# Kernel optimization log

Measured on AMD Instinct MI355X. Metric: run time of the kernel, lower is better.

## Reference

```python
import jax, jax.numpy as jnp
import numpy as np

EPS = 1e-5  # BatchNorm eps (eval mode, running stats mean=0, var=1)
BN_SCALE = 1.0 / np.sqrt(1.0 + EPS)


def setup_inputs() -> dict:
    key = jax.random.key(0)
    ks = jax.random.split(key, 5)
    N, T, C, V, K = 64, 300, 64, 25, 3
    x = jax.random.normal(ks[0], (N, T, C, V), dtype=jnp.float32)
    # G: Linear(T -> 2T, no bias), Linear(2T -> K, no bias)
    g_w1 = jax.random.normal(ks[1], (2 * T, T), dtype=jnp.float32) * (1.0 / np.sqrt(T))
    g_w2 = jax.random.normal(ks[2], (K, 2 * T), dtype=jnp.float32) * (1.0 / np.sqrt(2 * T))
    # L: Conv1d(C -> C//4, K, pad=K//2, no bias), Conv1d(C//4 -> C, 1, no bias)
    l_w1 = jax.random.normal(ks[3], (C // 4, C, K), dtype=jnp.float32) * (1.0 / np.sqrt(C * K))
    l_w2 = jax.random.normal(ks[4], (C, C // 4), dtype=jnp.float32) * (1.0 / np.sqrt(C // 4))
    return {"x": x, "g_w1": g_w1, "g_w2": g_w2, "l_w1": l_w1, "l_w2": l_w2}


def reference(x, g_w1, g_w2, l_w1, l_w2):
    # x: [N, T, C, V]; n_segment == T so n_batch == N
    N, T, C, V = x.shape
    K = g_w2.shape[0]
    pad = K // 2
    # new_x: [N, C, T, V]
    new_x = jnp.transpose(x, (0, 2, 1, 3))
    # adaptive avg pool over V -> [N, C, T]
    pooled = jnp.mean(new_x, axis=-1)

    # --- G branch: per-(n,c) temporal kernel of size K ---
    g_in = pooled.reshape(N * C, T)                         # [N*C, T]
    h = jnp.maximum(g_in @ g_w1.T * BN_SCALE, 0.0)          # Linear + BN(eval) + ReLU
    conv_kernel = jax.nn.softmax(h @ g_w2.T, axis=-1)       # [N*C, K]
    conv_kernel = conv_kernel.reshape(N, C, K)

    # --- L branch: local activation over time ---
    z = jax.lax.conv_general_dilated(
        pooled, l_w1, window_strides=(1,), padding=[(pad, pad)],
        dimension_numbers=("NCH", "OIH", "NCH"))              # [N, C//4, T]
    z = jnp.maximum(z * BN_SCALE, 0.0)
    local_act = jax.nn.sigmoid(jnp.einsum("nct,oc->not", z, l_w2))  # [N, C, T]

    new_x = new_x * local_act[..., None]                    # [N, C, T, V]

    # --- per-(n,c) depthwise temporal conv (groups = N*C) ---
    xpad = jnp.pad(new_x, ((0, 0), (0, 0), (pad, pad), (0, 0)))
    windows = jnp.stack([xpad[:, :, k:k + T, :] for k in range(K)], axis=-1)  # [N,C,T,V,K]
    out = jnp.einsum("nctvk,nck->nctv", windows, conv_kernel)

    return jnp.transpose(out, (0, 2, 1, 3))                 # [N, T, C, V]
```

## Files before the change

### kernel.cpp

```cpp
#include <hip/hip_runtime.h>
#include <hip/hip_bf16.h>
#include <math.h>

#define BN_SCALE_F 0.99999500003749969f

typedef short short8v __attribute__((ext_vector_type(8)));
typedef float float4v __attribute__((ext_vector_type(4)));


__global__ __launch_bounds__(256) void pool_prep_kernel(const float* __restrict__ x,
                                                        const float* __restrict__ g_w1,
                                                        const float* __restrict__ l_w1,
                                                        float* __restrict__ pooled,
                                                        __hip_bfloat16* __restrict__ pooledb,
                                                        __hip_bfloat16* __restrict__ w1b,
                                                        float* __restrict__ lw1r) {
  __shared__ float buf[6400];
  int bid = blockIdx.x;
  if (bid < 4800) {
    const float4* src = (const float4*)(x + (size_t)bid * 6400);
    float4* b4 = (float4*)buf;
    for (int i = threadIdx.x; i < 1600; i += 256) b4[i] = src[i];
    __syncthreads();
    int wave = threadIdx.x >> 6;
    int c = threadIdx.x & 63;
    int nt = bid * 4 + wave;
    int n = nt / 300, t = nt - n * 300;
    const float* p = buf + wave * 1600 + c * 25;
    float s = 0.f;
#pragma unroll
    for (int v = 0; v < 25; ++v) s += p[v];
    float pv = s * 0.04f;
    size_t row = (size_t)(n * 64 + c);
    pooled[row * 300 + t] = pv;
    pooledb[row * 320 + t] = __float2bfloat16(pv);
  } else if (bid < 4816) {
    int b = bid - 4800;
    for (int i = b * 256 + threadIdx.x; i < 608 * 320; i += 16 * 256) {
      int j = i / 320, k = i - j * 320;
      float v = (j < 600 && k < 300) ? g_w1[(size_t)j * 300 + k] : 0.f;
      w1b[i] = __float2bfloat16(v);
    }
  } else if (bid == 4816) {
    for (int i = threadIdx.x; i < 4096 * 20; i += 256) {
      int row = i / 20, k = 300 + (i - row * 20);
      pooledb[(size_t)row * 320 + k] = __float2bfloat16(0.f);
    }
  } else {
    for (int i = threadIdx.x; i < 3072; i += 256) {
      int o = i / 192;
      int rem = i - o * 192;
      int c = rem / 3;
      int k = rem - c * 3;
      lw1r[c * 48 + o * 3 + k] = l_w1[i];
    }
  }
}

union GLSmem {
  struct {
    float hbuf[16][612];
    float logits[48];
  } g;
  struct {
    float p[64][80];
    float z[75][20];
  } l;
};

__global__ __launch_bounds__(320) void gl_kernel(const float* __restrict__ pooled,
                                                 const __hip_bfloat16* __restrict__ pooledb,
                                                 const __hip_bfloat16* __restrict__ w1b,
                                                 const float* __restrict__ g_w2,
                                                 const float* __restrict__ lw1r,
                                                 const float* __restrict__ l_w2,
                                                 float* __restrict__ kern,
                                                 float* __restrict__ la) {
  __shared__ GLSmem sm;
  int bid = blockIdx.x;
  int tid = threadIdx.x;
  int wave = tid >> 6, lane = tid & 63;
  if (bid < 256) {
    int r0 = bid * 16;
    int row16 = lane & 15;
    int k8 = (lane >> 4) * 8;

    float4v acc[8];
#pragma unroll
    for (int q = 0; q < 8; ++q) acc[q] = (float4v){0.f, 0.f, 0.f, 0.f};

    const short* pa = (const short*)pooledb + (size_t)(r0 + row16) * 320 + k8;
    const short* pb = (const short*)w1b + k8;

    for (int kt = 0; kt < 10; ++kt) {
      short8v av = *(const short8v*)(pa + kt * 32);
#pragma unroll
      for (int q = 0; q < 8; ++q) {
        int jt = wave + 5 * q;
        if (jt < 38) {
          short8v bv = *(const short8v*)(pb + (size_t)(jt * 16 + row16) * 320 + kt * 32);
          acc[q] = __builtin_amdgcn_mfma_f32_16x16x32_bf16(av, bv, acc[q], 0, 0, 0);
        }
      }
    }

#pragma unroll
    for (int q = 0; q < 8; ++q) {
      int jt = wave + 5 * q;
      if (jt < 38) {
        int col = jt * 16 + row16;
#pragma unroll
        for (int reg = 0; reg < 4; ++reg) {
          int i = (lane >> 4) * 4 + reg;
          sm.g.hbuf[i][col] = fmaxf(acc[q][reg] * BN_SCALE_F, 0.f);
        }
      }
    }
    __syncthreads();

    for (int o = wave; o < 48; o += 5) {
      int r = o / 3, k = o - r * 3;
      float s = 0.f;
#pragma unroll
      for (int q = 0; q < 10; ++q) {
        int jj = lane + q * 64;
        if (jj < 600) s = fmaf(sm.g.hbuf[r][jj], g_w2[k * 600 + jj], s);
      }
#pragma unroll
      for (int off = 1; off < 64; off <<= 1) s += __shfl_xor(s, off, 64);
      if (lane == 0) sm.g.logits[o] = s;
    }
    __syncthreads();
    if (tid < 16) {
      float a = sm.g.logits[tid * 3 + 0];
      float b = sm.g.logits[tid * 3 + 1];
      float c = sm.g.logits[tid * 3 + 2];
      float m = fmaxf(a, fmaxf(b, c));
      float ea = expf(a - m), eb = expf(b - m), ec = expf(c - m);
      float inv = 1.f / (ea + eb + ec);
      size_t o = (size_t)(r0 + tid) * 3;
      kern[o] = ea * inv;
      kern[o + 1] = eb * inv;
      kern[o + 2] = ec * inv;
    }
  } else {
    int bid2 = bid - 256;
    int n = bid2 >> 2;
    int tc = bid2 & 3;
    int t0 = tc * 75;
    for (int i = tid; i < 64 * 77; i += 320) {
      int c = i / 77, tt = i - c * 77;
      int gt = t0 - 1 + tt;
      sm.l.p[c][tt] = (gt >= 0 && gt < 300) ? pooled[(size_t)(n * 64 + c) * 300 + gt] : 0.f;
    }
    __syncthreads();
    {
      int og = tid / 80;
      int tl = tid - og * 80;
      if (tl < 75) {
        float acc[4] = {0.f, 0.f, 0.f, 0.f};
        for (int c = 0; c < 64; ++c) {
          const float* wr = lw1r + c * 48 + og * 12;
          float pk0 = sm.l.p[c][tl];
          float pk1 = sm.l.p[c][tl + 1];
          float pk2 = sm.l.p[c][tl + 2];
#pragma unroll
          for (int oi = 0; oi < 4; ++oi) {
            acc[oi] = fmaf(wr[oi * 3 + 0], pk0, acc[oi]);
            acc[oi] = fmaf(wr[oi * 3 + 1], pk1, acc[oi]);
            acc[oi] = fmaf(wr[oi * 3 + 2], pk2, acc[oi]);
          }
        }
        float4 zv;
        zv.x = fmaxf(acc[0] * BN_SCALE_F, 0.f);
        zv.y = fmaxf(acc[1] * BN_SCALE_F, 0.f);
        zv.z = fmaxf(acc[2] * BN_SCALE_F, 0.f);
        zv.w = fmaxf(acc[3] * BN_SCALE_F, 0.f);
        *(float4*)(&sm.l.z[tl][og * 4]) = zv;
      }
    }
    __syncthreads();
    {
      int c = tid / 5;
      int ts = tid - c * 5;
      const float4* w2v = (const float4*)(l_w2 + c * 16);
      float4 wA = w2v[0], wB = w2v[1], wC = w2v[2], wD = w2v[3];
      float* outp = la + (size_t)(n * 64 + c) * 300 + t0;
      for (int it = 0; it < 15; ++it) {
        int tl = ts + it * 5;
        const float4* zv = (const float4*)(&sm.l.z[tl][0]);
        float4 zA = zv[0], zB = zv[1], zC = zv[2], zD = zv[3];
        float s = zA.x * wA.x + zA.y * wA.y + zA.z * wA.z + zA.w * wA.w;
        s += zB.x * wB.x + zB.y * wB.y + zB.z * wB.z + zB.w * wB.w;
        s += zC.x * wC.x + zC.y * wC.y + zC.z * wC.z + zC.w * wC.w;
        s += zD.x * wD.x + zD.y * wD.y + zD.z * wD.z + zD.w * wD.w;
        outp[tl] = 1.f / (1.f + expf(-s));
      }
    }
  }
}

__global__ __launch_bounds__(256) void tam_final_kernel(const float* __restrict__ x,
                                                        const float* __restrict__ la,
                                                        const float* __restrict__ kern,
                                                        float* __restrict__ out) {
  int bid = blockIdx.x;
  int n = bid >> 4;
  int rem = bid & 15;
  int tch = rem >> 1;
  int half = rem & 1;
  int cv4 = half * 256 + threadIdx.x;
  if (cv4 >= 400) return;
  int e0 = cv4 * 4;
  int c0 = e0 / 25;
  int c3 = (e0 + 3) / 25;
  bool s1 = ((e0 + 1) / 25) != c0;
  bool s2 = ((e0 + 2) / 25) != c0;
  bool s3 = (c3 != c0);
  const float* lap0 = la + (size_t)(n * 64 + c0) * 300;
  const float* lap1 = la + (size_t)(n * 64 + c3) * 300;
  const float* kp0 = kern + (size_t)(n * 64 + c0) * 3;
  const float* kp1 = kern + (size_t)(n * 64 + c3) * 3;
  float k00 = kp0[0], k01 = kp0[1], k02 = kp0[2];
  float k10 = kp1[0], k11 = kp1[1], k12 = kp1[2];
  float4 K0 = {k00, s1 ? k10 : k00, s2 ? k10 : k00, s3 ? k10 : k00};
  float4 K1 = {k01, s1 ? k11 : k01, s2 ? k11 : k01, s3 ? k11 : k01};
  float4 K2 = {k02, s1 ? k12 : k02, s2 ? k12 : k02, s3 ? k12 : k02};

  const float4* xp = (const float4*)(x + (size_t)n * 480000) + cv4;
  float4* op = (float4*)(out + (size_t)n * 480000) + cv4;

  int t0 = tch * 38;
  int tend = t0 + 38;
  if (tend > 300) tend = 300;

#define LAMUL(dst, t)                                        \
  {                                                          \
    float l0 = lap0[(t)];                                    \
    float l1 = lap1[(t)];                                    \
    float4 xv = xp[(size_t)(t) * 400];                       \
    dst.x = xv.x * l0;                                       \
    dst.y = xv.y * (s1 ? l1 : l0);                           \
    dst.z = xv.z * (s2 ? l1 : l0);                           \
    dst.w = xv.w * (s3 ? l1 : l0);                           \
  }

  float4 am, ac, an;
  if (t0 > 0) {
    LAMUL(am, t0 - 1);
  } else {
    am = {0.f, 0.f, 0.f, 0.f};
  }
  LAMUL(ac, t0);
  for (int t = t0; t < tend; ++t) {
    if (t + 1 < 300) {
      LAMUL(an, t + 1);
    } else {
      an = {0.f, 0.f, 0.f, 0.f};
    }
    float4 o;
    o.x = fmaf(am.x, K0.x, fmaf(ac.x, K1.x, an.x * K2.x));
    o.y = fmaf(am.y, K0.y, fmaf(ac.y, K1.y, an.y * K2.y));
    o.z = fmaf(am.z, K0.z, fmaf(ac.z, K1.z, an.z * K2.z));
    o.w = fmaf(am.w, K0.w, fmaf(ac.w, K1.w, an.w * K2.w));
    op[(size_t)t * 400] = o;
    am = ac;
    ac = an;
  }
#undef LAMUL
}

extern "C" void kernel_launch(void* const* d_in, const int* in_sizes, int n_in,
                              void* d_out, int out_size, void* d_ws, size_t ws_size,
                              hipStream_t stream) {
  const float* x = (const float*)d_in[0];
  const float* g_w1 = (const float*)d_in[1];
  const float* g_w2 = (const float*)d_in[2];
  const float* l_w1 = (const float*)d_in[3];
  const float* l_w2 = (const float*)d_in[4];
  float* out = (float*)d_out;
  float* ws = (float*)d_ws;
  float* pooled = ws;
  float* kern = ws + 1228800;
  float* lact = ws + 1228800 + 12288;
  __hip_bfloat16* pooledb = (__hip_bfloat16*)(ws + 2469888);
  __hip_bfloat16* w1b = (__hip_bfloat16*)(ws + 2469888 + 655360);
  float* lw1r = ws + 2469888 + 655360 + 97280;

  hipLaunchKernelGGL(pool_prep_kernel, dim3(4818), dim3(256), 0, stream, x, g_w1, l_w1,
                     pooled, pooledb, w1b, lw1r);
  hipLaunchKernelGGL(gl_kernel, dim3(512), dim3(320), 0, stream, pooled, pooledb, w1b,
                     g_w2, lw1r, l_w2, kern, lact);
  hipLaunchKernelGGL(tam_final_kernel, dim3(1024), dim3(256), 0, stream, x, lact, kern, out);
}
```

Measured before the change: 121.2 us.

## Write pooled activations in time-major layout and transpose to bf16 in separate kernel

The pooling kernel now writes pooled values contiguously as [N,T,C] (coalesced across channels) instead of strided scatter stores into [N*C,T] fp32 and bf16 buffers. A new prep kernel transposes this through shared memory into the padded bf16 layout used by the G-branch matmul, zeroing the pad columns as part of the tile. It also converts the weights. The L branch reads the time-major layout directly, and its shared tile is padded to 81 columns to avoid bank conflicts. This targets uncoalesced global stores, at the cost of an extra kernel launch and an extra pass over the pooled data.

Result: faster. 112.3 us (-7.3%).

```diff
diff --git a/kernel.cpp b/kernel.cpp
--- a/kernel.cpp
+++ b/kernel.cpp
@@ -8,43 +8,50 @@
 typedef float float4v __attribute__((ext_vector_type(4)));
 
 
-__global__ __launch_bounds__(256) void pool_prep_kernel(const float* __restrict__ x,
-                                                        const float* __restrict__ g_w1,
-                                                        const float* __restrict__ l_w1,
-                                                        float* __restrict__ pooled,
-                                                        __hip_bfloat16* __restrict__ pooledb,
-                                                        __hip_bfloat16* __restrict__ w1b,
-                                                        float* __restrict__ lw1r) {
+__global__ __launch_bounds__(256) void pool_kernel(const float* __restrict__ x,
+                                                   float* __restrict__ pooledT) {
   __shared__ float buf[6400];
   int bid = blockIdx.x;
-  if (bid < 4800) {
-    const float4* src = (const float4*)(x + (size_t)bid * 6400);
-    float4* b4 = (float4*)buf;
-    for (int i = threadIdx.x; i < 1600; i += 256) b4[i] = src[i];
-    __syncthreads();
-    int wave = threadIdx.x >> 6;
-    int c = threadIdx.x & 63;
-    int nt = bid * 4 + wave;
-    int n = nt / 300, t = nt - n * 300;
-    const float* p = buf + wave * 1600 + c * 25;
-    float s = 0.f;
-#pragma unroll
-    for (int v = 0; v < 25; ++v) s += p[v];
-    float pv = s * 0.04f;
-    size_t row = (size_t)(n * 64 + c);
-    pooled[row * 300 + t] = pv;
-    pooledb[row * 320 + t] = __float2bfloat16(pv);
-  } else if (bid < 4816) {
-    int b = bid - 4800;
+  const float4* src = (const float4*)(x + (size_t)bid * 6400);
+  float4* b4 = (float4*)buf;
+  for (int i = threadIdx.x; i < 1600; i += 256) b4[i] = src[i];
+  __syncthreads();
+  int wave = threadIdx.x >> 6;
+  int c = threadIdx.x & 63;
+  const float* p = buf + wave * 1600 + c * 25;
+  float s = 0.f;
+#pragma unroll
+  for (int v = 0; v < 25; ++v) s += p[v];
+  pooledT[(size_t)(bid * 4 + wave) * 64 + c] = s * 0.04f;
+}
+
+__global__ __launch_bounds__(256) void prep2_kernel(const float* __restrict__ pooledT,
+                                                    const float* __restrict__ g_w1,
+                                                    const float* __restrict__ l_w1,
+                                                    __hip_bfloat16* __restrict__ pooledb,
+                                                    __hip_bfloat16* __restrict__ w1b,
+                                                    float* __restrict__ lw1r) {
+  int bid = blockIdx.x;
+  if (bid < 320) {
+    __shared__ float tile[64][65];
+    int n = bid / 5;
+    int tt0 = (bid % 5) * 64;
+    for (int i = threadIdx.x; i < 4096; i += 256) {
+      int tt = i >> 6, c = i & 63;
+      int t = tt0 + tt;
+      tile[tt][c] = (t < 300) ? pooledT[((size_t)n * 300 + t) * 64 + c] : 0.f;
+    }
+    __syncthreads();
+    for (int i = threadIdx.x; i < 4096; i += 256) {
+      int c = i >> 6, tt = i & 63;
+      pooledb[((size_t)(n * 64 + c)) * 320 + tt0 + tt] = __float2bfloat16(tile[tt][c]);
+    }
+  } else if (bid < 336) {
+    int b = bid - 320;
     for (int i = b * 256 + threadIdx.x; i < 608 * 320; i += 16 * 256) {
       int j = i / 320, k = i - j * 320;
       float v = (j < 600 && k < 300) ? g_w1[(size_t)j * 300 + k] : 0.f;
       w1b[i] = __float2bfloat16(v);
-    }
-  } else if (bid == 4816) {
-    for (int i = threadIdx.x; i < 4096 * 20; i += 256) {
-      int row = i / 20, k = 300 + (i - row * 20);
-      pooledb[(size_t)row * 320 + k] = __float2bfloat16(0.f);
     }
   } else {
     for (int i = threadIdx.x; i < 3072; i += 256) {
@@ -63,12 +70,12 @@
     float logits[48];
   } g;
   struct {
-    float p[64][80];
+    float p[64][81];
     float z[75][20];
   } l;
 };
 
-__global__ __launch_bounds__(320) void gl_kernel(const float* __restrict__ pooled,
+__global__ __launch_bounds__(320) void gl_kernel(const float* __restrict__ pooledT,
                                                  const __hip_bfloat16* __restrict__ pooledb,
                                                  const __hip_bfloat16* __restrict__ w1b,
                                                  const float* __restrict__ g_w2,
@@ -148,10 +155,10 @@
     int n = bid2 >> 2;
     int tc = bid2 & 3;
     int t0 = tc * 75;
-    for (int i = tid; i < 64 * 77; i += 320) {
-      int c = i / 77, tt = i - c * 77;
+    for (int i = tid; i < 77 * 64; i += 320) {
+      int tt = i >> 6, c = i & 63;
       int gt = t0 - 1 + tt;
-      sm.l.p[c][tt] = (gt >= 0 && gt < 300) ? pooled[(size_t)(n * 64 + c) * 300 + gt] : 0.f;
+      sm.l.p[c][tt] = (gt >= 0 && gt < 300) ? pooledT[((size_t)n * 300 + gt) * 64 + c] : 0.f;
     }
     __syncthreads();
     {
@@ -280,16 +287,17 @@
   const float* l_w2 = (const float*)d_in[4];
   float* out = (float*)d_out;
   float* ws = (float*)d_ws;
-  float* pooled = ws;
+  float* pooledT = ws;
   float* kern = ws + 1228800;
   float* lact = ws + 1228800 + 12288;
   __hip_bfloat16* pooledb = (__hip_bfloat16*)(ws + 2469888);
   __hip_bfloat16* w1b = (__hip_bfloat16*)(ws + 2469888 + 655360);
   float* lw1r = ws + 2469888 + 655360 + 97280;
 
-  hipLaunchKernelGGL(pool_prep_kernel, dim3(4818), dim3(256), 0, stream, x, g_w1, l_w1,
-                     pooled, pooledb, w1b, lw1r);
-  hipLaunchKernelGGL(gl_kernel, dim3(512), dim3(320), 0, stream, pooled, pooledb, w1b,
+  hipLaunchKernelGGL(pool_kernel, dim3(4800), dim3(256), 0, stream, x, pooledT);
+  hipLaunchKernelGGL(prep2_kernel, dim3(337), dim3(256), 0, stream, pooledT, g_w1, l_w1,
+                     pooledb, w1b, lw1r);
+  hipLaunchKernelGGL(gl_kernel, dim3(512), dim3(320), 0, stream, pooledT, pooledb, w1b,
                      g_w2, lw1r, l_w2, kern, lact);
   hipLaunchKernelGGL(tam_final_kernel, dim3(1024), dim3(256), 0, stream, x, lact, kern, out);
 }
```
